# Kernel optimization log

Hardware: AMD Instinct MI355X
Metric: run time of the kernel (lower is better)

The kernel has to match this reference:

```python
import jax, jax.numpy as jnp
import numpy as np

NUM_CLASSES = 41
EPS = 1e-12


def nearest_resize(lab, h, w):
    # torch F.interpolate(mode='nearest'): src_idx = floor(dst_idx * in / out)
    Hl, Wl = lab.shape[1], lab.shape[2]
    ih = (jnp.arange(h) * Hl) // h
    iw = (jnp.arange(w) * Wl) // w
    return lab[:, ih][:, :, iw]


def segment_mean(feats, lab_small, base):
    # feats [b,c,h,w], lab_small [b,h,w] int, base [b,L,c] (values for absent labels)
    b, c, h, w = feats.shape
    L = NUM_CLASSES
    lab = lab_small.reshape(b, h * w)
    ids = (jnp.arange(b, dtype=lab.dtype)[:, None] * L + lab).reshape(-1)  # [b*h*w]
    x = feats.reshape(b, c, h * w).transpose(0, 2, 1).reshape(-1, c)       # [b*h*w, c]
    sums = jax.ops.segment_sum(x, ids, num_segments=b * L).reshape(b, L, c)
    cnts = jax.ops.segment_sum(jnp.ones((b * h * w,), feats.dtype), ids,
                               num_segments=b * L).reshape(b, L, 1)
    mean = sums / jnp.maximum(cnts, 1.0)
    return jnp.where(cnts > 0, mean, base)


def ra_gate(feats, lab_small, base, w1, w2):
    # RA.forward: segment-mean queue -> L2 normalize over class dim -> sum -> 1x1 convs -> sigmoid
    att = segment_mean(feats, lab_small, base)                      # [b,L,c]
    nrm = jnp.sqrt(jnp.sum(att * att, axis=1, keepdims=True))       # over classes (dim=1)
    att = att / jnp.maximum(nrm, EPS)
    s = jnp.sum(att, axis=1)                                        # [b,c]
    h1 = jax.nn.relu(jnp.einsum('bc,oc->bo', s, w1))                # conv1 1x1, no bias
    g = jax.nn.sigmoid(jnp.einsum('bo,co->bc', h1, w2))             # conv2 1x1, no bias
    return g[:, :, None, None]                                      # [b,c,1,1]


def conv3x3(x, w):
    return jax.lax.conv_general_dilated(
        x, w, window_strides=(1, 1), padding=((1, 1), (1, 1)),
        dimension_numbers=('NCHW', 'OIHW', 'NCHW'))


def setup_inputs() -> dict:
    key = jax.random.key(0)
    ks = jax.random.split(key, 10)
    B, C, H, W = 8, 128, 128, 128
    return {
        'r': jax.random.normal(ks[0], (B, C, H, W), jnp.float32),
        'd': jax.random.normal(ks[1], (B, C, H, W), jnp.float32),
        'label': jax.random.randint(ks[2], (B, 4 * H, 4 * W), 0, NUM_CLASSES, jnp.int32),
        'conv_w': jax.random.normal(ks[3], (C, 2 * C, 3, 3), jnp.float32) * 0.05,
        'f_w1': jax.random.normal(ks[4], (C // 16, C), jnp.float32) * 0.05,
        'f_w2': jax.random.normal(ks[5], (C, C // 16), jnp.float32) * 0.05,
        'd_w1': jax.random.normal(ks[6], (C // 16, C), jnp.float32) * 0.05,
        'd_w2': jax.random.normal(ks[7], (C, C // 16), jnp.float32) * 0.05,
        'seg_base_f': jax.random.normal(ks[8], (B, NUM_CLASSES, C), jnp.float32),
        'seg_base_d': jax.random.normal(ks[9], (B, NUM_CLASSES, C), jnp.float32),
    }


def reference(r, d, label, conv_w, f_w1, f_w2, d_w1, d_w2, seg_base_f, seg_base_d):
    b, c, h, w = r.shape
    add = r + d
    mul = r * jax.nn.sigmoid(d)
    fuse = conv3x3(jnp.concatenate([add, mul], axis=1), conv_w)
    lab_small = nearest_resize(label, h, w)
    d_ra = d * ra_gate(d, lab_small, seg_base_d, d_w1, d_w2)
    fuse_ra = fuse * ra_gate(fuse, lab_small, seg_base_f, f_w1, f_w2)
    return fuse_ra + d_ra
```

## Files before the change

### kernel.cpp

```cpp
#include <hip/hip_runtime.h>
#include <math.h>

typedef unsigned short u16;
typedef unsigned char u8;
typedef unsigned int u32;
typedef unsigned long long u64;
typedef __bf16 bf16x8 __attribute__((ext_vector_type(8)));
typedef float f32x4 __attribute__((ext_vector_type(4)));

#define NL 41
#define HW 16384

#define NHWC_OFF   0
#define WA_OFF     67108864
#define LAB8_OFF   67698688
#define GHIST_OFF  67829760
#define ISUM_OFF   67831808
#define GATES_OFF  68503552

__device__ __forceinline__ u16 f2bf(float f) {
    u32 u = __builtin_bit_cast(u32, f);
    u = (u + 0x7FFFu + ((u >> 16) & 1u)) >> 16;
    return (u16)u;
}

__device__ __forceinline__ void glds16(const void* g, void* l) {
    __builtin_amdgcn_global_load_lds(
        (const __attribute__((address_space(1))) void*)g,
        (__attribute__((address_space(3))) void*)l, 16, 0, 0);
}

#define ISUM_SCALE 4294967296.f
#define ISUM_INV   2.3283064365386963e-10f

__global__ __launch_bounds__(64)
void k_wpack(const float* __restrict__ w, u16* __restrict__ wa,
             int* __restrict__ ghist, u64* __restrict__ isum)
{
    const int bid = (int)blockIdx.x;
    const int l = (int)threadIdx.x;
    if (bid == 0) {
        for (int i = l; i < 8 * NL; i += 64) ghist[i] = 0;
    }
    if (bid < 64) {
        u64* p = isum + bid * 1312;
        for (int i = l; i < 1312; i += 64) p[i] = 0ull;
    }
    const int kt = bid >> 3, ct = bid & 7;
    const int chunk = kt / 9, tap = kt - chunk * 9;
    const int co = ct * 16 + (l & 15);
    const int cin0 = chunk * 32 + (l >> 4) * 8;
    u16 tmp[8];
#pragma unroll
    for (int j = 0; j < 8; ++j)
        tmp[j] = f2bf(w[((size_t)co * 256 + cin0 + j) * 9 + tap]);
    *(f32x4*)&wa[((size_t)bid * 64 + l) * 8] = *(f32x4*)tmp;
}

__global__ __launch_bounds__(256, 2)
void k_prep(const float* __restrict__ r, const float* __restrict__ d,
            const int* __restrict__ label, u16* __restrict__ nhwc,
            u8* __restrict__ lab8, int* __restrict__ ghist,
            u64* __restrict__ isum_d)
{
    __shared__ u16 s[64 * 256];
    __shared__ float binsd[NL * 256];
    __shared__ int hist[NL];
    __shared__ u8 s_lab[256];
    const int bid = (int)blockIdx.x;
    const int b = bid >> 6;
    const int px0 = (bid & 63) * 256;
    const int tid = (int)threadIdx.x;
    const int c = tid & 127;
    const int half = tid >> 7;

    if (tid < NL) hist[tid] = 0;
    for (int i = tid; i < NL * 64; i += 256) ((f32x4*)binsd)[i] = f32x4{0,0,0,0};
    __syncthreads();

    {
        int px = px0 + tid;
        int yy = px >> 7, xx = px & 127;
        int lab = label[(size_t)b * 512 * 512 + (yy * 4) * 512 + xx * 4];
        lab8[b * HW + px] = (u8)lab;
        s_lab[tid] = (u8)lab;
        atomicAdd(&hist[lab], 1);
    }
    __syncthreads();

    for (int t = 0; t < 4; ++t) {
        const int pxb = px0 + t * 64 + half * 32;
        const float* rp = r + ((size_t)(b * 128 + c)) * HW + pxb;
        const float* dp = d + ((size_t)(b * 128 + c)) * HW + pxb;
        const u8* lp = &s_lab[t * 64 + half * 32];
        uint4 lw0 = *(const uint4*)lp;
        uint4 lw1 = *(const uint4*)(lp + 16);
        u32 lwords[8] = {lw0.x, lw0.y, lw0.z, lw0.w, lw1.x, lw1.y, lw1.z, lw1.w};
#pragma unroll
        for (int j = 0; j < 8; ++j) {
            float4 rv = *(const float4*)(rp + j * 4);
            float4 dv = *(const float4*)(dp + j * 4);
            float ra[4] = {rv.x, rv.y, rv.z, rv.w};
            float da[4] = {dv.x, dv.y, dv.z, dv.w};
#pragma unroll
            for (int i = 0; i < 4; ++i) {
                int pxl = half * 32 + j * 4 + i;
                s[pxl * 256 + c] = f2bf(ra[i] + da[i]);
                s[pxl * 256 + 128 + c] = f2bf(ra[i] / (1.f + __expf(-da[i])));
                int lab = (int)((lwords[j] >> (i * 8)) & 0xffu);
                binsd[lab * 256 + tid] += da[i];
            }
        }
        __syncthreads();
        const f32x4* sf = (const f32x4*)s;
        f32x4* dst = (f32x4*)nhwc + ((size_t)b * HW + px0 + t * 64) * 32;
#pragma unroll
        for (int k = 0; k < 8; ++k) {
            int fi = k * 256 + tid;
            dst[fi] = sf[fi];
        }
        __syncthreads();
    }
    for (int i = tid; i < NL * 128; i += 256) {
        int lab = i >> 7, cc = i & 127;
        float v = binsd[lab * 256 + cc] + binsd[lab * 256 + 128 + cc];
        if (v != 0.f) {
            long long q = (long long)(v * ISUM_SCALE);
            atomicAdd(&isum_d[(b * NL + lab) * 128 + cc], (u64)q);
        }
    }
    if (tid < NL && hist[tid] > 0) atomicAdd(&ghist[b * NL + tid], hist[tid]);
}

__global__ __launch_bounds__(256, 2)
void k_conv(const u16* __restrict__ nhwc, const u16* __restrict__ wa,
            const u8* __restrict__ lab8, float* __restrict__ out,
            u64* __restrict__ isum_f)
{
    __shared__ u16 s_in[2 * 2080 * 8];
    __shared__ u8 s_lab[256];
    const int tid = (int)threadIdx.x;
    const int bid = (int)blockIdx.x;
    const int b = bid & 7;
    const int y0 = (bid >> 3) * 2;
    const int l = tid & 63;
    const int wv = tid >> 6;
    const int wr = wv & 1;
    const int wc = wv >> 1;
    const int l15 = l & 15;
    const int l16 = l >> 4;

    {
        f32x4 zz = {0.f, 0.f, 0.f, 0.f};
        for (int i = tid; i < 4160; i += 256) ((f32x4*)s_in)[i] = zz;
    }
    s_lab[tid] = lab8[b * HW + y0 * 128 + tid];

    int goff[9];
#pragma unroll
    for (int it = 0; it < 9; ++it) {
        int s = it * 256 + tid;
        int row = s / 520;
        int rem = s - row * 520;
        int xslot = rem >> 2;
        int ci8 = rem & 3;
        int gy = y0 - 1 + row;
        int gx = xslot - 1;
        bool valid = (s < 2080) && ((unsigned)gy < 128u) && ((unsigned)gx < 128u);
        goff[it] = valid ? (((gy << 7) | gx) * 256 + ci8 * 8) * 2 : -1;
    }

    f32x4 acc[4][8];
#pragma unroll
    for (int i = 0; i < 4; ++i)
#pragma unroll
        for (int j = 0; j < 8; ++j) {
            f32x4 zz = {0.f, 0.f, 0.f, 0.f};
            acc[i][j] = zz;
        }

    const char* src_b = (const char*)(nhwc + (size_t)b * HW * 256);
    const int lane_base = (tid & 192) * 16;
    const f32x4* wa4 = (const f32x4*)wa;

    __syncthreads();
#pragma unroll
    for (int it = 0; it < 9; ++it)
        if (goff[it] >= 0)
            glds16(src_b + goff[it], (char*)s_in + it * 4096 + lane_base);

#pragma unroll 1
    for (int chunk = 0; chunk < 8; ++chunk) {
        __syncthreads();

        f32x4 a0[4], a1[4];
        {
            int kt8 = chunk * 72;
#pragma unroll
            for (int i = 0; i < 4; ++i) a0[i] = wa4[(kt8 + wc * 4 + i) * 64 + l];
#pragma unroll
            for (int i = 0; i < 4; ++i) a1[i] = wa4[(kt8 + 8 + wc * 4 + i) * 64 + l];
        }
        if (chunk < 7) {
            char* dstb = (char*)s_in + ((chunk + 1) & 1) * 33280 + lane_base;
#pragma unroll
            for (int it = 0; it < 9; ++it)
                if (goff[it] >= 0)
                    glds16(src_b + goff[it] + (chunk + 1) * 64, dstb + it * 4096);
        }

        const char* bufp = (const char*)s_in + (chunk & 1) * 33280;
#pragma unroll
        for (int tap = 0; tap < 9; ++tap) {
            f32x4 aC[4];
#pragma unroll
            for (int i = 0; i < 4; ++i) aC[i] = a0[i];
#pragma unroll
            for (int i = 0; i < 4; ++i) a0[i] = a1[i];
            if (tap + 2 < 9) {
                int kt8 = chunk * 72 + (tap + 2) * 8;
#pragma unroll
                for (int i = 0; i < 4; ++i)
                    a1[i] = wa4[(kt8 + wc * 4 + i) * 64 + l];
            }
            const int rowi = wr + tap / 3;
            const int dxo = tap % 3;
            f32x4 bf[8];
#pragma unroll
            for (int p = 0; p < 8; ++p) {
                int e = (rowi * 130 + p * 16 + l15 + dxo) * 64 + l16 * 16;
                bf[p] = *(const f32x4*)(bufp + e);
            }
#pragma unroll
            for (int ct = 0; ct < 4; ++ct) {
                bf16x8 av = __builtin_bit_cast(bf16x8, aC[ct]);
#pragma unroll
                for (int p = 0; p < 8; ++p)
                    acc[ct][p] = __builtin_amdgcn_mfma_f32_16x16x32_bf16(
                        av, __builtin_bit_cast(bf16x8, bf[p]), acc[ct][p], 0, 0, 0);
            }
        }
    }

    const int y = y0 + wr;
    float* outb = out + (size_t)b * 128 * HW + (size_t)y * 128;
#pragma unroll
    for (int ct = 0; ct < 4; ++ct)
#pragma unroll
        for (int p = 0; p < 8; ++p) {
            int x = p * 16 + l15;
#pragma unroll
            for (int rr = 0; rr < 4; ++rr) {
                int co = wc * 64 + ct * 16 + l16 * 4 + rr;
                outb[(size_t)co * HW + x] = acc[ct][p][rr];
            }
        }

    __syncthreads();
    float* binsf = (float*)s_in;
    for (int i = tid; i < NL * 133; i += 256) binsf[i] = 0.f;
    __syncthreads();
#pragma unroll
    for (int ct = 0; ct < 4; ++ct)
#pragma unroll
        for (int p = 0; p < 8; ++p) {
            int lab = (int)s_lab[wr * 128 + p * 16 + l15];
            float* bp = &binsf[lab * 133 + wc * 64 + ct * 16 + l16 * 4];
#pragma unroll
            for (int rr = 0; rr < 4; ++rr)
                atomicAdd(bp + rr, acc[ct][p][rr]);
        }
    __syncthreads();
    for (int i = tid; i < NL * 128; i += 256) {
        int lab = i >> 7, cc = i & 127;
        float v = binsf[lab * 133 + cc];
        if (v != 0.f) {
            long long q = (long long)(v * ISUM_SCALE);
            atomicAdd(&isum_f[(b * NL + lab) * 128 + cc], (u64)q);
        }
    }
}

__global__ __launch_bounds__(128)
void k_gates(const u64* __restrict__ isum, const int* __restrict__ ghist,
             const float* __restrict__ base_f, const float* __restrict__ base_d,
             const float* __restrict__ f_w1, const float* __restrict__ f_w2,
             const float* __restrict__ d_w1, const float* __restrict__ d_w2,
             float* __restrict__ gates)
{
    __shared__ float sv[128];
    __shared__ float h1[8];
    const int b = (int)blockIdx.x >> 1;
    const int feat = (int)blockIdx.x & 1;
    const int c = (int)threadIdx.x;

    const float* base = feat ? base_d : base_f;
    float suma = 0.f, sumsq = 0.f;
    for (int lc = 0; lc < NL; ++lc) {
        long long q = (long long)isum[((size_t)(feat * 8 + b) * NL + lc) * 128 + c];
        float s = (float)q * ISUM_INV;
        int cnt = ghist[b * NL + lc];
        float att = (cnt > 0) ? (s / (float)cnt) : base[(b * NL + lc) * 128 + c];
        suma += att;
        sumsq += att * att;
    }
    sv[c] = suma / fmaxf(sqrtf(sumsq), 1e-12f);
    __syncthreads();

    const float* w1 = feat ? d_w1 : f_w1;
    const float* w2 = feat ? d_w2 : f_w2;
    if (c < 8) {
        float h = 0.f;
        for (int k = 0; k < 128; ++k) h += w1[c * 128 + k] * sv[k];
        h1[c] = fmaxf(h, 0.f);
    }
    __syncthreads();

    float gv = 0.f;
#pragma unroll
    for (int o = 0; o < 8; ++o) gv += w2[c * 8 + o] * h1[o];
    gates[feat * 1024 + b * 128 + c] = 1.f / (1.f + expf(-gv));
}

__global__ __launch_bounds__(256)
void k_final(const float* __restrict__ d, const float* __restrict__ gates,
             float* out)
{
    size_t t4 = (size_t)blockIdx.x * 256 + threadIdx.x;
    size_t basei = t4 * 4;
    int bc = (int)(basei >> 14);
    float gf = gates[bc];
    float gd = gates[1024 + bc];
    float4 f = *(const float4*)(out + basei);
    float4 dv = *(const float4*)(d + basei);
    float4 o;
    o.x = f.x * gf + dv.x * gd;
    o.y = f.y * gf + dv.y * gd;
    o.z = f.z * gf + dv.z * gd;
    o.w = f.w * gf + dv.w * gd;
    *(float4*)(out + basei) = o;
}

extern "C" void kernel_launch(void* const* d_in, const int* in_sizes, int n_in,
                              void* d_out, int out_size, void* d_ws, size_t ws_size,
                              hipStream_t stream)
{
    (void)in_sizes; (void)n_in; (void)out_size; (void)ws_size;
    const float* r      = (const float*)d_in[0];
    const float* d      = (const float*)d_in[1];
    const int*   label  = (const int*)d_in[2];
    const float* conv_w = (const float*)d_in[3];
    const float* f_w1   = (const float*)d_in[4];
    const float* f_w2   = (const float*)d_in[5];
    const float* d_w1   = (const float*)d_in[6];
    const float* d_w2   = (const float*)d_in[7];
    const float* base_f = (const float*)d_in[8];
    const float* base_d = (const float*)d_in[9];
    float* out = (float*)d_out;

    char* ws = (char*)d_ws;
    u16* nhwc    = (u16*)(ws + NHWC_OFF);
    u16* wa      = (u16*)(ws + WA_OFF);
    u8*  lab8    = (u8*)(ws + LAB8_OFF);
    int* ghist   = (int*)(ws + GHIST_OFF);
    u64* isum    = (u64*)(ws + ISUM_OFF);
    u64* isum_f  = isum;
    u64* isum_d  = isum + 8 * NL * 128;
    float* gates = (float*)(ws + GATES_OFF);

    hipLaunchKernelGGL(k_wpack, dim3(576), dim3(64), 0, stream, conv_w, wa,
                       ghist, isum);
    hipLaunchKernelGGL(k_prep, dim3(512), dim3(256), 0, stream, r, d, label,
                       nhwc, lab8, ghist, isum_d);
    hipLaunchKernelGGL(k_conv, dim3(512), dim3(256), 0, stream, nhwc, wa,
                       lab8, out, isum_f);
    hipLaunchKernelGGL(k_gates, dim3(16), dim3(128), 0, stream, isum, ghist,
                       base_f, base_d, f_w1, f_w2, d_w1, d_w2, gates);
    hipLaunchKernelGGL(k_final, dim3(16384), dim3(256), 0, stream, d, gates, out);
}
```

Before: 429.9 us.

## Replace global 64-bit atomic segment sums with per-block partials and reduction kernels

Per-block label/channel segment sums for d and fuse are no longer accumulated through fixed-point 64-bit global atomics. They are written as float partial arrays and summed by a separate k_red kernel. The conv epilogue now uses two per-row LDS bin sets to cut LDS atomic contention. When the workspace is too small, the conv epilogue is skipped and a standalone k_seg_f pass re-reads the fuse output instead. This removes global atomic contention and the zeroing pass, at the cost of extra launches and partial-buffer traffic, and the d partials are staged in the output buffer.

```diff
diff --git a/kernel.cpp b/kernel.cpp
--- a/kernel.cpp
+++ b/kernel.cpp
@@ -15,8 +15,12 @@
 #define WA_OFF     67108864
 #define LAB8_OFF   67698688
 #define GHIST_OFF  67829760
-#define ISUM_OFF   67831808
-#define GATES_OFF  68503552
+#define SUMS_OFF   67833856
+#define GATES_OFF  68169728
+#define PF_OFF     68177920
+#define PF_END     78925824ull
+
+#define PSZ 5248
 
 __device__ __forceinline__ u16 f2bf(float f) {
     u32 u = __builtin_bit_cast(u32, f);
@@ -30,21 +34,14 @@
         (__attribute__((address_space(3))) void*)l, 16, 0, 0);
 }
 
-#define ISUM_SCALE 4294967296.f
-#define ISUM_INV   2.3283064365386963e-10f
-
 __global__ __launch_bounds__(64)
 void k_wpack(const float* __restrict__ w, u16* __restrict__ wa,
-             int* __restrict__ ghist, u64* __restrict__ isum)
+             int* __restrict__ ghist)
 {
     const int bid = (int)blockIdx.x;
     const int l = (int)threadIdx.x;
     if (bid == 0) {
         for (int i = l; i < 8 * NL; i += 64) ghist[i] = 0;
-    }
-    if (bid < 64) {
-        u64* p = isum + bid * 1312;
-        for (int i = l; i < 1312; i += 64) p[i] = 0ull;
     }
     const int kt = bid >> 3, ct = bid & 7;
     const int chunk = kt / 9, tap = kt - chunk * 9;
@@ -61,7 +58,7 @@
 void k_prep(const float* __restrict__ r, const float* __restrict__ d,
             const int* __restrict__ label, u16* __restrict__ nhwc,
             u8* __restrict__ lab8, int* __restrict__ ghist,
-            u64* __restrict__ isum_d)
+            float* __restrict__ pd)
 {
     __shared__ u16 s[64 * 256];
     __shared__ float binsd[NL * 256];
@@ -121,21 +118,19 @@
         }
         __syncthreads();
     }
+    float* pout = pd + (size_t)bid * PSZ;
     for (int i = tid; i < NL * 128; i += 256) {
         int lab = i >> 7, cc = i & 127;
-        float v = binsd[lab * 256 + cc] + binsd[lab * 256 + 128 + cc];
-        if (v != 0.f) {
-            long long q = (long long)(v * ISUM_SCALE);
-            atomicAdd(&isum_d[(b * NL + lab) * 128 + cc], (u64)q);
-        }
+        pout[i] = binsd[lab * 256 + cc] + binsd[lab * 256 + 128 + cc];
     }
     if (tid < NL && hist[tid] > 0) atomicAdd(&ghist[b * NL + tid], hist[tid]);
 }
 
+template<int EP>
 __global__ __launch_bounds__(256, 2)
 void k_conv(const u16* __restrict__ nhwc, const u16* __restrict__ wa,
             const u8* __restrict__ lab8, float* __restrict__ out,
-            u64* __restrict__ isum_f)
+            float* __restrict__ pf)
 {
     __shared__ u16 s_in[2 * 2080 * 8];
     __shared__ u8 s_lab[256];
@@ -154,7 +149,7 @@
         f32x4 zz = {0.f, 0.f, 0.f, 0.f};
         for (int i = tid; i < 4160; i += 256) ((f32x4*)s_in)[i] = zz;
     }
-    s_lab[tid] = lab8[b * HW + y0 * 128 + tid];
+    if (EP) s_lab[tid] = lab8[b * HW + y0 * 128 + tid];
 
     int goff[9];
 #pragma unroll
@@ -256,33 +251,86 @@
             }
         }
 
-    __syncthreads();
-    float* binsf = (float*)s_in;
-    for (int i = tid; i < NL * 133; i += 256) binsf[i] = 0.f;
-    __syncthreads();
-#pragma unroll
-    for (int ct = 0; ct < 4; ++ct)
-#pragma unroll
-        for (int p = 0; p < 8; ++p) {
-            int lab = (int)s_lab[wr * 128 + p * 16 + l15];
-            float* bp = &binsf[lab * 133 + wc * 64 + ct * 16 + l16 * 4];
-#pragma unroll
-            for (int rr = 0; rr < 4; ++rr)
-                atomicAdd(bp + rr, acc[ct][p][rr]);
-        }
-    __syncthreads();
-    for (int i = tid; i < NL * 128; i += 256) {
-        int lab = i >> 7, cc = i & 127;
-        float v = binsf[lab * 133 + cc];
-        if (v != 0.f) {
-            long long q = (long long)(v * ISUM_SCALE);
-            atomicAdd(&isum_f[(b * NL + lab) * 128 + cc], (u64)q);
+    if (EP) {
+        __syncthreads();
+        float* binsf = (float*)s_in;
+        for (int i = tid; i < 2 * NL * 129; i += 256) binsf[i] = 0.f;
+        __syncthreads();
+#pragma unroll
+        for (int ct = 0; ct < 4; ++ct)
+#pragma unroll
+            for (int p = 0; p < 8; ++p) {
+                int lab = (int)s_lab[wr * 128 + p * 16 + l15];
+                float* bp = &binsf[(wr * NL + lab) * 129 + wc * 64 + ct * 16 + l16 * 4];
+#pragma unroll
+                for (int rr = 0; rr < 4; ++rr)
+                    atomicAdd(bp + rr, acc[ct][p][rr]);
+            }
+        __syncthreads();
+        float* pout = pf + (size_t)bid * PSZ;
+        for (int i = tid; i < NL * 128; i += 256) {
+            int lab = i >> 7, cc = i & 127;
+            pout[i] = binsf[lab * 129 + cc] + binsf[(NL + lab) * 129 + cc];
         }
     }
 }
 
 __global__ __launch_bounds__(128)
-void k_gates(const u64* __restrict__ isum, const int* __restrict__ ghist,
+void k_red(const float* __restrict__ p, float* __restrict__ sout,
+           int bstride, int kstride)
+{
+    const int bid = (int)blockIdx.x;
+    const int b = bid / 41, lab = bid - b * 41;
+    const int c = (int)threadIdx.x;
+    const float* q = p + (size_t)b * bstride + lab * 128 + c;
+    float s = 0.f;
+#pragma unroll 8
+    for (int k = 0; k < 64; ++k) s += q[(size_t)k * kstride];
+    sout[(size_t)bid * 128 + c] = s;
+}
+
+__global__ __launch_bounds__(256, 3)
+void k_seg_f(const float* __restrict__ fuse, const u8* __restrict__ lab8,
+             float* __restrict__ sums)
+{
+    __shared__ float bins[NL][256];
+    const int bid = (int)blockIdx.x;
+    const int c = bid & 127;
+    const int b = bid >> 7;
+    const int tid = (int)threadIdx.x;
+
+    for (int i = tid; i < NL * 256; i += 256) ((float*)bins)[i] = 0.f;
+    __syncthreads();
+
+    const float* src = fuse + ((size_t)(b * 128 + c)) * HW;
+    const u8* lp = lab8 + b * HW;
+
+#pragma unroll 4
+    for (int k = 0; k < 16; ++k) {
+        int i = k * 256 + tid;
+        float4 v = ((const float4*)src)[i];
+        uchar4 lv = ((const uchar4*)lp)[i];
+        bins[lv.x][tid] += v.x;
+        bins[lv.y][tid] += v.y;
+        bins[lv.z][tid] += v.z;
+        bins[lv.w][tid] += v.w;
+    }
+    __syncthreads();
+
+    for (int stride = 128; stride >= 1; stride >>= 1) {
+        for (int idx = tid; idx < NL * stride; idx += 256) {
+            int l = idx / stride;
+            int cc = idx - l * stride;
+            bins[l][cc] += bins[l][cc + stride];
+        }
+        __syncthreads();
+    }
+    if (tid < NL)
+        sums[(size_t)(b * NL + tid) * 128 + c] = bins[tid][0];
+}
+
+__global__ __launch_bounds__(128)
+void k_gates(const float* __restrict__ sums, const int* __restrict__ ghist,
              const float* __restrict__ base_f, const float* __restrict__ base_d,
              const float* __restrict__ f_w1, const float* __restrict__ f_w2,
              const float* __restrict__ d_w1, const float* __restrict__ d_w2,
@@ -295,10 +343,10 @@
     const int c = (int)threadIdx.x;
 
     const float* base = feat ? base_d : base_f;
+    const float* sf = sums + (size_t)feat * 8 * NL * 128;
     float suma = 0.f, sumsq = 0.f;
     for (int lc = 0; lc < NL; ++lc) {
-        long long q = (long long)isum[((size_t)(feat * 8 + b) * NL + lc) * 128 + c];
-        float s = (float)q * ISUM_INV;
+        float s = sf[(size_t)(b * NL + lc) * 128 + c];
         int cnt = ghist[b * NL + lc];
         float att = (cnt > 0) ? (s / (float)cnt) : base[(b * NL + lc) * 128 + c];
         suma += att;
@@ -345,7 +393,7 @@
                               void* d_out, int out_size, void* d_ws, size_t ws_size,
                               hipStream_t stream)
 {
-    (void)in_sizes; (void)n_in; (void)out_size; (void)ws_size;
+    (void)in_sizes; (void)n_in; (void)out_size;
     const float* r      = (const float*)d_in[0];
     const float* d      = (const float*)d_in[1];
     const int*   label  = (const int*)d_in[2];
@@ -363,18 +411,32 @@
     u16* wa      = (u16*)(ws + WA_OFF);
     u8*  lab8    = (u8*)(ws + LAB8_OFF);
     int* ghist   = (int*)(ws + GHIST_OFF);
-    u64* isum    = (u64*)(ws + ISUM_OFF);
-    u64* isum_f  = isum;
-    u64* isum_d  = isum + 8 * NL * 128;
+    float* sums  = (float*)(ws + SUMS_OFF);
+    float* sums_f = sums;
+    float* sums_d = sums + 8 * NL * 128;
     float* gates = (float*)(ws + GATES_OFF);
-
-    hipLaunchKernelGGL(k_wpack, dim3(576), dim3(64), 0, stream, conv_w, wa,
-                       ghist, isum);
+    float* pf    = (float*)(ws + PF_OFF);
+    float* pd    = (float*)d_out;
+
+    const bool big = ws_size >= PF_END;
+
+    hipLaunchKernelGGL(k_wpack, dim3(576), dim3(64), 0, stream, conv_w, wa, ghist);
     hipLaunchKernelGGL(k_prep, dim3(512), dim3(256), 0, stream, r, d, label,
-                       nhwc, lab8, ghist, isum_d);
-    hipLaunchKernelGGL(k_conv, dim3(512), dim3(256), 0, stream, nhwc, wa,
-                       lab8, out, isum_f);
-    hipLaunchKernelGGL(k_gates, dim3(16), dim3(128), 0, stream, isum, ghist,
+                       nhwc, lab8, ghist, pd);
+    hipLaunchKernelGGL(k_red, dim3(328), dim3(128), 0, stream, pd, sums_d,
+                       64 * PSZ, PSZ);
+    if (big) {
+        hipLaunchKernelGGL(k_conv<1>, dim3(512), dim3(256), 0, stream, nhwc, wa,
+                           lab8, out, pf);
+        hipLaunchKernelGGL(k_red, dim3(328), dim3(128), 0, stream, pf, sums_f,
+                           PSZ, 8 * PSZ);
+    } else {
+        hipLaunchKernelGGL(k_conv<0>, dim3(512), dim3(256), 0, stream, nhwc, wa,
+                           lab8, out, (float*)nullptr);
+        hipLaunchKernelGGL(k_seg_f, dim3(1024), dim3(256), 0, stream, out,
+                           lab8, sums_f);
+    }
+    hipLaunchKernelGGL(k_gates, dim3(16), dim3(128), 0, stream, sums, ghist,
                        base_f, base_d, f_w1, f_w2, d_w1, d_w2, gates);
     hipLaunchKernelGGL(k_final, dim3(16384), dim3(256), 0, stream, d, gates, out);
 }
```

Measured after the change: 428.8 us. About the same (-0.3%).
